# Optimization experiments

Hardware: AMD Instinct MI355X
Metric: run time of the kernel (lower is better)

The kernel has to match this reference:

```python
import jax, jax.numpy as jnp
import numpy as np

EPS = 1e-5      # BatchNorm eps (torch default)
TEMP = 2.0      # initial_temperature
TOP_K = 2


def _bn(x, g, b, m, v):
    # eval-mode BatchNorm over channel dim of [B, C]
    return (x - m) * jax.lax.rsqrt(v + EPS) * g + b


def setup_inputs() -> dict:
    key = jax.random.key(0)
    ks = jax.random.split(key, 16)
    B, C, H, W, E = 64, 768, 32, 32, 16
    C2 = 2 * C            # 1536
    R = C2 // 16          # 96 (ChannelAttention bottleneck)
    s = 0.02
    f32 = jnp.float32
    return {
        "x": jax.random.normal(ks[0], (B, C, H, W), f32),
        # conv1x1 C->2C
        "w1": jax.random.normal(ks[1], (C2, C), f32) * s,
        "b1": jnp.zeros((C2,), f32),
        # BN(2C)
        "bn1_g": jnp.ones((C2,), f32),
        "bn1_b": jnp.zeros((C2,), f32),
        "bn1_m": jax.random.normal(ks[2], (C2,), f32) * 0.1,
        "bn1_v": jax.random.uniform(ks[3], (C2,), f32, 0.5, 1.5),
        # ChannelAttention fc: 2C -> 2C/16 -> 2C
        "caw1": jax.random.normal(ks[4], (R, C2), f32) * s,
        "cab1": jnp.zeros((R,), f32),
        "caw2": jax.random.normal(ks[5], (C2, R), f32) * s,
        "cab2": jnp.zeros((C2,), f32),
        # conv1x1 2C->C
        "w2": jax.random.normal(ks[6], (C, C2), f32) * s,
        "b2": jnp.zeros((C,), f32),
        # BN(C)
        "bn2_g": jnp.ones((C,), f32),
        "bn2_b": jnp.zeros((C,), f32),
        "bn2_m": jax.random.normal(ks[7], (C,), f32) * 0.1,
        "bn2_v": jax.random.uniform(ks[8], (C,), f32, 0.5, 1.5),
        # conv1x1 C->E
        "w3": jax.random.normal(ks[9], (E, C), f32) * s,
        "b3": jnp.zeros((E,), f32),
    }


def reference(x, w1, b1, bn1_g, bn1_b, bn1_m, bn1_v,
              caw1, cab1, caw2, cab2,
              w2, b2, bn2_g, bn2_b, bn2_m, bn2_v,
              w3, b3):
    # global avg pool: [B,C,H,W] -> [B,C] (1x1 spatial squeezed)
    g = jnp.mean(x, axis=(2, 3))
    # conv1x1 C->2C + BN + GELU (exact erf gelu, torch default)
    h = jax.nn.gelu(_bn(g @ w1.T + b1, bn1_g, bn1_b, bn1_m, bn1_v),
                    approximate=False)
    # ChannelAttention on 1x1 feature map: avg_pool == max_pool == identity,
    # so avg_out + max_out = 2 * fc(h)
    a = jax.nn.gelu(h @ caw1.T + cab1, approximate=False) @ caw2.T + cab2
    h = h * jax.nn.sigmoid(a + a)
    # conv1x1 2C->C + BN + GELU
    h = jax.nn.gelu(_bn(h @ w2.T + b2, bn2_g, bn2_b, bn2_m, bn2_v),
                    approximate=False)
    # conv1x1 C->E -> gating scores [B, E]
    scores = h @ w3.T + b3
    vals, idx = jax.lax.top_k(scores, TOP_K)
    probs = jax.nn.softmax(vals / TEMP, axis=1)
    return idx, probs
```

## Files before the change

### kernel.cpp

```cpp
#include <hip/hip_runtime.h>
#include <hip/hip_bf16.h>
#include <math.h>

#define B_   64
#define C_   768
#define C2_  1536
#define R_   96
#define E_   16
#define HW_  1024

__device__ __forceinline__ float gelu_exact(float x) {
    return 0.5f * x * (1.0f + erff(x * 0.70710678118654752440f));
}

__global__ __launch_bounds__(256) void pool_kernel(const float* __restrict__ x,
                                                   float* __restrict__ gT) {
    const int wave = threadIdx.x >> 6;
    const int lane = threadIdx.x & 63;
    const int row  = blockIdx.x * 4 + wave;
    const int b = row / C_;
    const int c = row % C_;
    const float4* p = reinterpret_cast<const float4*>(x + (size_t)row * HW_);
    float4 a0 = p[lane +   0];
    float4 a1 = p[lane +  64];
    float4 a2 = p[lane + 128];
    float4 a3 = p[lane + 192];
    float s = (a0.x + a0.y + a0.z + a0.w) + (a1.x + a1.y + a1.z + a1.w)
            + (a2.x + a2.y + a2.z + a2.w) + (a3.x + a3.y + a3.z + a3.w);
    #pragma unroll
    for (int off = 32; off >= 1; off >>= 1) s += __shfl_xor(s, off);
    if (lane == 0) gT[c * B_ + b] = s * (1.0f / (float)HW_);
}

template<int K, bool BN>
__global__ __launch_bounds__(512) void gemv2_kernel(
    const float* __restrict__ inT,
    const float* __restrict__ W,
    const float* __restrict__ bias,
    const float* __restrict__ bn_g, const float* __restrict__ bn_b,
    const float* __restrict__ bn_m, const float* __restrict__ bn_v,
    float* __restrict__ outT)
{
    __shared__ __align__(16) float wl[2 * K];
    __shared__ float part[2][8][64];
    const int t  = threadIdx.x;
    const int c0 = blockIdx.x * 2;
    {
        const float4* src = reinterpret_cast<const float4*>(W + (size_t)c0 * K);
        float4* dst = reinterpret_cast<float4*>(wl);
        #pragma unroll
        for (int i = t; i < K / 2; i += 512) dst[i] = src[i];
    }
    __syncthreads();
    const int b = t & 63, w = t >> 6;
    const int kc = w * (K / 8);
    const float* w0 = wl + kc;
    const float* w1 = wl + K + kc;
    const float* g  = inT + (size_t)kc * B_ + b;
    float a0 = 0.f, a1 = 0.f;
    #pragma unroll 16
    for (int k = 0; k < K / 8; ++k) {
        float gv = g[k * B_];
        a0 = fmaf(gv, w0[k], a0);
        a1 = fmaf(gv, w1[k], a1);
    }
    part[0][w][b] = a0;
    part[1][w][b] = a1;
    __syncthreads();
    if (t < 128) {
        const int ci = t >> 6, bb = t & 63, c = c0 + ci;
        float s = (part[ci][0][bb] + part[ci][1][bb])
                + (part[ci][2][bb] + part[ci][3][bb])
                + (part[ci][4][bb] + part[ci][5][bb])
                + (part[ci][6][bb] + part[ci][7][bb]);
        s += bias[c];
        if (BN) s = (s - bn_m[c]) * rsqrtf(bn_v[c] + 1e-5f) * bn_g[c] + bn_b[c];
        outT[(size_t)c * B_ + bb] = gelu_exact(s);
    }
}

__global__ __launch_bounds__(512) void gate_kernel(
    const float* __restrict__ rT,
    const float* __restrict__ caw2,
    const float* __restrict__ cab2,
    float* __restrict__ h1T)
{
    const int t = threadIdx.x;
    const int b = t & 63, w = t >> 6;
    const int c = blockIdx.x * 8 + w;
    const float* wr = caw2 + (size_t)c * R_;
    float acc = 0.f;
    #pragma unroll 12
    for (int k = 0; k < R_; ++k) acc = fmaf(rT[k * B_ + b], wr[k], acc);
    acc += cab2[c];
    float sig = 1.0f / (1.0f + expf(-2.0f * acc));
    h1T[(size_t)c * B_ + b] *= sig;
}

__global__ __launch_bounds__(256) void l5_kernel(
    const float* __restrict__ h2T, const float* __restrict__ w3,
    const float* __restrict__ b3, float* __restrict__ out)
{
    __shared__ __align__(16) float wl[E_ * C_];
    __shared__ float part[256];
    __shared__ float sc[E_];
    const int t = threadIdx.x;
    const int b = blockIdx.x;
    {
        const float4* src = reinterpret_cast<const float4*>(w3);
        float4* dst = reinterpret_cast<float4*>(wl);
        #pragma unroll
        for (int i = 0; i < 12; ++i) dst[t + 256 * i] = src[t + 256 * i];
    }
    __syncthreads();
    const int e = t & 15, kg = t >> 4;
    const float* wr = wl + e * C_ + kg * 48;
    const float* hv = h2T + (size_t)kg * 48 * B_ + b;
    float acc = 0.f;
    #pragma unroll 8
    for (int j = 0; j < 48; ++j) acc = fmaf(hv[j * B_], wr[j], acc);
    part[t] = acc;
    __syncthreads();
    if (t < E_) {
        float s = b3[t];
        #pragma unroll
        for (int kgi = 0; kgi < 16; ++kgi) s += part[kgi * 16 + t];
        sc[t] = s;
    }
    __syncthreads();
    if (t == 0) {
        int i0 = 0; float v0 = sc[0];
        #pragma unroll
        for (int i = 1; i < E_; ++i) { if (sc[i] > v0) { v0 = sc[i]; i0 = i; } }
        int i1 = -1; float v1 = -INFINITY;
        #pragma unroll
        for (int i = 0; i < E_; ++i) {
            if (i == i0) continue;
            if (sc[i] > v1) { v1 = sc[i]; i1 = i; }
        }
        float e1 = expf((v1 - v0) * 0.5f);
        float inv = 1.0f / (1.0f + e1);
        out[b * 2 + 0] = (float)i0;
        out[b * 2 + 1] = (float)i1;
        out[2 * B_ + b * 2 + 0] = inv;
        out[2 * B_ + b * 2 + 1] = e1 * inv;
    }
}

extern "C" void kernel_launch(void* const* d_in, const int* in_sizes, int n_in,
                              void* d_out, int out_size, void* d_ws, size_t ws_size,
                              hipStream_t stream) {
    const float* x     = (const float*)d_in[0];
    const float* w1    = (const float*)d_in[1];
    const float* b1    = (const float*)d_in[2];
    const float* bn1_g = (const float*)d_in[3];
    const float* bn1_b = (const float*)d_in[4];
    const float* bn1_m = (const float*)d_in[5];
    const float* bn1_v = (const float*)d_in[6];
    const float* caw1  = (const float*)d_in[7];
    const float* cab1  = (const float*)d_in[8];
    const float* caw2  = (const float*)d_in[9];
    const float* cab2  = (const float*)d_in[10];
    const float* w2    = (const float*)d_in[11];
    const float* b2    = (const float*)d_in[12];
    const float* bn2_g = (const float*)d_in[13];
    const float* bn2_b = (const float*)d_in[14];
    const float* bn2_m = (const float*)d_in[15];
    const float* bn2_v = (const float*)d_in[16];
    const float* w3    = (const float*)d_in[17];
    const float* b3    = (const float*)d_in[18];

    float* ws  = (float*)d_ws;
    float* gT  = ws;
    float* h1T = ws + 49152;
    float* rT  = ws + 49152 + 98304;
    float* h2T = ws + 49152 + 98304 + 6144;
    float* out = (float*)d_out;

    pool_kernel<<<(B_ * C_) / 4, 256, 0, stream>>>(x, gT);
    gemv2_kernel<C_, true><<<C2_ / 2, 512, 0, stream>>>(
        gT, w1, b1, bn1_g, bn1_b, bn1_m, bn1_v, h1T);
    gemv2_kernel<C2_, false><<<R_ / 2, 512, 0, stream>>>(
        h1T, caw1, cab1, nullptr, nullptr, nullptr, nullptr, rT);
    gate_kernel<<<C2_ / 8, 512, 0, stream>>>(rT, caw2, cab2, h1T);
    gemv2_kernel<C2_, true><<<C_ / 2, 512, 0, stream>>>(
        h1T, w2, b2, bn2_g, bn2_b, bn2_m, bn2_v, h2T);
    l5_kernel<<<B_, 256, 0, stream>>>(h2T, w3, b3, out);
}
```

Measured before the change: 72.22 us.

## Use nontemporal pool loads, split small GEMVs, drop LDS staging in l5

The pool kernel now reads x with nontemporal vector loads so the 200MB streaming read does not pollute cache. The channel-attention first layer gets a dedicated kernel with one output channel per block (96 blocks instead of 48) and three independent accumulators. The gate kernel splits its reduction into two chains, makes the channel index wave-uniform, and writes the gated result to a separate buffer instead of updating in place. l5 reads w3 directly from global memory rather than staging 48KB in LDS. These are several small independent tweaks. Nearly all the time is spent in the bandwidth-bound pool kernel, so the effect hinges on whether the nontemporal hint changes its achieved bandwidth.

Measured after the change: 66.97 us. 7.3% less time.

```diff
diff --git a/kernel.cpp b/kernel.cpp
--- a/kernel.cpp
+++ b/kernel.cpp
@@ -8,6 +8,8 @@
 #define R_   96
 #define E_   16
 #define HW_  1024
+
+typedef float f32x4 __attribute__((ext_vector_type(4)));
 
 __device__ __forceinline__ float gelu_exact(float x) {
     return 0.5f * x * (1.0f + erff(x * 0.70710678118654752440f));
@@ -20,11 +22,11 @@
     const int row  = blockIdx.x * 4 + wave;
     const int b = row / C_;
     const int c = row % C_;
-    const float4* p = reinterpret_cast<const float4*>(x + (size_t)row * HW_);
-    float4 a0 = p[lane +   0];
-    float4 a1 = p[lane +  64];
-    float4 a2 = p[lane + 128];
-    float4 a3 = p[lane + 192];
+    const f32x4* p = reinterpret_cast<const f32x4*>(x + (size_t)row * HW_);
+    f32x4 a0 = __builtin_nontemporal_load(p + lane +   0);
+    f32x4 a1 = __builtin_nontemporal_load(p + lane +  64);
+    f32x4 a2 = __builtin_nontemporal_load(p + lane + 128);
+    f32x4 a3 = __builtin_nontemporal_load(p + lane + 192);
     float s = (a0.x + a0.y + a0.z + a0.w) + (a1.x + a1.y + a1.z + a1.w)
             + (a2.x + a2.y + a2.z + a2.w) + (a3.x + a3.y + a3.z + a3.w);
     #pragma unroll
@@ -79,42 +81,71 @@
     }
 }
 
+__global__ __launch_bounds__(512) void l2_kernel(
+    const float* __restrict__ h1T, const float* __restrict__ caw1,
+    const float* __restrict__ cab1, float* __restrict__ rT)
+{
+    __shared__ __align__(16) float wl[C2_];
+    __shared__ float part[8][64];
+    const int t = threadIdx.x;
+    const int c = blockIdx.x;
+    {
+        const float4* src = reinterpret_cast<const float4*>(caw1 + (size_t)c * C2_);
+        float4* dst = reinterpret_cast<float4*>(wl);
+        if (t < 384) dst[t] = src[t];
+    }
+    __syncthreads();
+    const int b = t & 63, w = t >> 6;
+    const int kc = w * 192;
+    const float* hp = h1T + (size_t)kc * B_ + b;
+    float a0 = 0.f, a1 = 0.f, a2 = 0.f;
+    #pragma unroll 8
+    for (int k = 0; k < 64; ++k) {
+        a0 = fmaf(hp[k * B_],         wl[kc + k],       a0);
+        a1 = fmaf(hp[(k + 64) * B_],  wl[kc + k + 64],  a1);
+        a2 = fmaf(hp[(k + 128) * B_], wl[kc + k + 128], a2);
+    }
+    part[w][b] = (a0 + a1) + a2;
+    __syncthreads();
+    if (t < 64) {
+        float s = 0.f;
+        #pragma unroll
+        for (int ww = 0; ww < 8; ++ww) s += part[ww][t];
+        rT[(size_t)c * B_ + t] = gelu_exact(s + cab1[c]);
+    }
+}
+
 __global__ __launch_bounds__(512) void gate_kernel(
-    const float* __restrict__ rT,
-    const float* __restrict__ caw2,
+    const float* __restrict__ rT, const float* __restrict__ caw2,
     const float* __restrict__ cab2,
-    float* __restrict__ h1T)
+    const float* __restrict__ h1T, float* __restrict__ h1gT)
 {
     const int t = threadIdx.x;
     const int b = t & 63, w = t >> 6;
-    const int c = blockIdx.x * 8 + w;
+    const int c = __builtin_amdgcn_readfirstlane(blockIdx.x * 8 + w);
     const float* wr = caw2 + (size_t)c * R_;
-    float acc = 0.f;
-    #pragma unroll 12
-    for (int k = 0; k < R_; ++k) acc = fmaf(rT[k * B_ + b], wr[k], acc);
-    acc += cab2[c];
-    float sig = 1.0f / (1.0f + expf(-2.0f * acc));
-    h1T[(size_t)c * B_ + b] *= sig;
+    const float* rp = rT + b;
+    float a0 = 0.f, a1 = 0.f;
+    #pragma unroll 8
+    for (int k = 0; k < 48; ++k) {
+        a0 = fmaf(rp[k * B_],        wr[k],      a0);
+        a1 = fmaf(rp[(k + 48) * B_], wr[k + 48], a1);
+    }
+    float a = a0 + a1 + cab2[c];
+    float sig = 1.0f / (1.0f + expf(-2.0f * a));
+    h1gT[(size_t)c * B_ + b] = h1T[(size_t)c * B_ + b] * sig;
 }
 
 __global__ __launch_bounds__(256) void l5_kernel(
     const float* __restrict__ h2T, const float* __restrict__ w3,
     const float* __restrict__ b3, float* __restrict__ out)
 {
-    __shared__ __align__(16) float wl[E_ * C_];
     __shared__ float part[256];
     __shared__ float sc[E_];
     const int t = threadIdx.x;
     const int b = blockIdx.x;
-    {
-        const float4* src = reinterpret_cast<const float4*>(w3);
-        float4* dst = reinterpret_cast<float4*>(wl);
-        #pragma unroll
-        for (int i = 0; i < 12; ++i) dst[t + 256 * i] = src[t + 256 * i];
-    }
-    __syncthreads();
     const int e = t & 15, kg = t >> 4;
-    const float* wr = wl + e * C_ + kg * 48;
+    const float* wr = w3 + (size_t)e * C_ + kg * 48;
     const float* hv = h2T + (size_t)kg * 48 * B_ + b;
     float acc = 0.f;
     #pragma unroll 8
@@ -170,20 +201,20 @@
     const float* w3    = (const float*)d_in[17];
     const float* b3    = (const float*)d_in[18];
 
-    float* ws  = (float*)d_ws;
-    float* gT  = ws;
-    float* h1T = ws + 49152;
-    float* rT  = ws + 49152 + 98304;
-    float* h2T = ws + 49152 + 98304 + 6144;
+    float* ws   = (float*)d_ws;
+    float* gT   = ws;
+    float* h1T  = ws + 49152;
+    float* rT   = ws + 147456;
+    float* h2T  = ws + 153600;
+    float* h1gT = ws + 202752;
     float* out = (float*)d_out;
 
     pool_kernel<<<(B_ * C_) / 4, 256, 0, stream>>>(x, gT);
     gemv2_kernel<C_, true><<<C2_ / 2, 512, 0, stream>>>(
         gT, w1, b1, bn1_g, bn1_b, bn1_m, bn1_v, h1T);
-    gemv2_kernel<C2_, false><<<R_ / 2, 512, 0, stream>>>(
-        h1T, caw1, cab1, nullptr, nullptr, nullptr, nullptr, rT);
-    gate_kernel<<<C2_ / 8, 512, 0, stream>>>(rT, caw2, cab2, h1T);
+    l2_kernel<<<R_, 512, 0, stream>>>(h1T, caw1, cab1, rT);
+    gate_kernel<<<C2_ / 8, 512, 0, stream>>>(rT, caw2, cab2, h1T, h1gT);
     gemv2_kernel<C2_, true><<<C_ / 2, 512, 0, stream>>>(
-        h1T, w2, b2, bn2_g, bn2_b, bn2_m, bn2_v, h2T);
+        h1gT, w2, b2, bn2_g, bn2_b, bn2_m, bn2_v, h2T);
     l5_kernel<<<B_, 256, 0, stream>>>(h2T, w3, b3, out);
 }
```
